# Kernel tuning notes

Measured on AMD Instinct MI355X. Metric: run time of the kernel, lower is better.

The kernel has to match this reference:

```python
import jax, jax.numpy as jnp
import numpy as np

B, C, H, W = 4, 256, 48, 48
HEADS, DH = 8, 32
INNER = HEADS * DH
HID = 128  # max(16, INNER//2)
SCALE = DH ** -0.5
EPS = 1e-6


def setup_inputs() -> dict:
    key = jax.random.key(0)
    ks = jax.random.split(key, 32)
    s = 0.02
    inp = {
        'x': jax.random.normal(ks[0], (B, C, H, W), jnp.float32),
        'rgb_input': jax.random.uniform(ks[1], (B, 3, H, W), jnp.float32),
        'wq': jax.random.normal(ks[2], (INNER, C), jnp.float32) * s,
        'bq': jnp.zeros((INNER,), jnp.float32),
        'wk': jax.random.normal(ks[3], (INNER, C), jnp.float32) * s,
        'bk': jnp.zeros((INNER,), jnp.float32),
        'wv': jax.random.normal(ks[4], (INNER, C), jnp.float32) * s,
        'bv': jnp.zeros((INNER,), jnp.float32),
        'wproj': jax.random.normal(ks[5], (C, INNER), jnp.float32) * s,
        'bproj': jnp.zeros((C,), jnp.float32),
        'c1_w': jax.random.normal(ks[6], (HID, 1, 3, 3), jnp.float32) * s,
        'c1_b': jnp.zeros((HID,), jnp.float32),
        'c2_w': jax.random.normal(ks[7], (HID, HID, 3, 3), jnp.float32) * s,
        'c2_b': jnp.zeros((HID,), jnp.float32),
        'gq_w': jax.random.normal(ks[8], (INNER, HID), jnp.float32) * s,
        'gq_b': jnp.ones((INNER,), jnp.float32),
        'bqf_w': jax.random.normal(ks[9], (INNER, HID), jnp.float32) * s,
        'bqf_b': jnp.zeros((INNER,), jnp.float32),
        'gk_w': jax.random.normal(ks[10], (INNER, HID), jnp.float32) * s,
        'gk_b': jnp.ones((INNER,), jnp.float32),
        'bkf_w': jax.random.normal(ks[11], (INNER, HID), jnp.float32) * s,
        'bkf_b': jnp.zeros((INNER,), jnp.float32),
        'gv_w': jax.random.normal(ks[12], (INNER, HID), jnp.float32) * s,
        'gv_b': jnp.ones((INNER,), jnp.float32),
        'bvf_w': jax.random.normal(ks[13], (INNER, HID), jnp.float32) * s,
        'bvf_b': jnp.zeros((INNER,), jnp.float32),
        'alpha': jnp.float32(0.1),
    }
    return inp


def _conv3(x, w, b):
    y = jax.lax.conv_general_dilated(x, w, (1, 1), 'SAME',
                                     dimension_numbers=('NCHW', 'OIHW', 'NCHW'))
    return y + b[None, :, None, None]


def _rgb_to_luma(rgb):
    y = 0.299 * rgb[:, 0:1] + 0.587 * rgb[:, 1:2] + 0.114 * rgb[:, 2:3]
    y_min = jnp.min(y, axis=(2, 3), keepdims=True)
    y_max = jnp.max(y, axis=(2, 3), keepdims=True)
    return (y - y_min) / (y_max - y_min + EPS)


def reference(x, rgb_input, wq, bq, wk, bk, wv, bv, wproj, bproj,
              c1_w, c1_b, c2_w, c2_b,
              gq_w, gq_b, bqf_w, bqf_b, gk_w, gk_b, bkf_w, bkf_b,
              gv_w, gv_b, bvf_w, bvf_b, alpha):
    Bx, Cx, Hx, Wx = x.shape
    N = Hx * Wx
    luma = _rgb_to_luma(rgb_input)  # [B,1,H,W]

    # LumaCond trunk + FiLM params (1x1 convs then global spatial mean)
    h = jax.nn.relu(_conv3(luma, c1_w, c1_b))
    h = jax.nn.relu(_conv3(h, c2_w, c2_b))
    hm = h.mean(axis=(2, 3))  # [B,HID] (mean commutes with 1x1 conv)

    def film_params(gw, gb, bw, bb):
        g = hm @ gw.T + gb  # [B, INNER]
        bta = hm @ bw.T + bb
        return (g.reshape(Bx, HEADS, DH, 1), bta.reshape(Bx, HEADS, DH, 1))

    gq, fbq = film_params(gq_w, gq_b, bqf_w, bqf_b)
    gk, fbk = film_params(gk_w, gk_b, bkf_w, bkf_b)
    gv, fbv = film_params(gv_w, gv_b, bvf_w, bvf_b)

    def proj_film(w, b, g, bta):
        t = jnp.einsum('bchw,oc->bohw', x, w) + b[None, :, None, None]
        t = t.reshape(Bx, HEADS, DH, N)
        return g * t + bta  # [B,heads,dh,N]

    q = proj_film(wq, bq, gq, fbq)
    k = proj_film(wk, bk, gk, fbk)
    v = proj_film(wv, bv, gv, fbv)

    logits = jnp.einsum('bhdn,bhdm->bhnm', q, k) * SCALE  # [B,heads,N,N]

    # luma bias: avg-pooled inverse luma, mean-centered per image
    invL = 1.0 - luma
    invL = jax.lax.reduce_window(invL, 0.0, jax.lax.add,
                                 (1, 1, 3, 3), (1, 1, 1, 1), 'SAME') / 9.0
    invL = invL.reshape(Bx, N)
    invL = invL - invL.mean(axis=-1, keepdims=True)
    logits = logits + alpha * invL[:, None, None, :]

    attn = jax.nn.softmax(logits, axis=-1)
    out = jnp.einsum('bhnm,bhdm->bhdn', attn, v)  # [B,heads,dh,N]
    out = out.reshape(Bx, INNER, Hx, Wx)
    return jnp.einsum('bchw,oc->bohw', out, wproj) + bproj[None, :, None, None]
```

## Files before the change

### kernel.cpp

```cpp
#include <hip/hip_runtime.h>


#define NSP 2304
#define WID 48

typedef __attribute__((ext_vector_type(4))) float  fvec4;
typedef __attribute__((ext_vector_type(2))) unsigned int uvec2;
typedef __attribute__((ext_vector_type(4))) unsigned int uvec4;
typedef __attribute__((ext_vector_type(8))) short  short8;
typedef __attribute__((ext_vector_type(4))) float  f32x4;

__device__ inline unsigned short f2bf(float f){
  unsigned int u = __builtin_bit_cast(unsigned int, f);
  u += 0x7fffu + ((u >> 16) & 1u);
  return (unsigned short)(u >> 16);
}
__device__ inline unsigned pack2bf(float a, float b){
#if __has_builtin(__builtin_amdgcn_cvt_pk_bf16_f32)
  typedef __attribute__((ext_vector_type(2))) __bf16 bf16x2;
  bf16x2 r = __builtin_amdgcn_cvt_pk_bf16_f32(a, b);
  return __builtin_bit_cast(unsigned, r);
#else
  return (unsigned)f2bf(a) | ((unsigned)f2bf(b) << 16);
#endif
}

__global__ void k0b_wcast(const float* __restrict__ c2w, const float* __restrict__ wq,
                          const float* __restrict__ wk, const float* __restrict__ wv_,
                          const float* __restrict__ wproj,
                          unsigned short* __restrict__ wtb,
                          unsigned short* __restrict__ wqkvb,
                          unsigned short* __restrict__ wprojb){
  int idx = blockIdx.x*256 + threadIdx.x;
  if (idx < 147456){
    int ic = idx & 127, rem = idx >> 7;
    int oc = rem & 127, tap = rem >> 7;
    wtb[idx] = f2bf(c2w[(oc*128 + ic)*9 + tap]);
  } else if (idx < 344064){
    int j = idx - 147456;
    int mat = j >> 16, oc_ = j & 65535;
    const float* src = (mat == 0) ? wq : (mat == 1) ? wk : wv_;
    wqkvb[j] = f2bf(src[oc_]);
  } else {
    int j = idx - 344064;
    wprojb[j] = f2bf(wproj[j]);
  }
}

__global__ __launch_bounds__(256) void k0xt(const float* __restrict__ x,
                                            unsigned short* __restrict__ xt){
  int nt = blockIdx.x, cc = blockIdx.y, b = blockIdx.z, t = threadIdx.x;
  __shared__ unsigned short tb[64*72];
  int cl0 = t >> 4;
  int nl0 = (t & 15) * 4;
  #pragma unroll
  for (int ps = 0; ps < 4; ++ps){
    int cl = cl0 + ps*16;
    fvec4 v = *(const fvec4*)(x + ((size_t)(b*256 + cc*64 + cl))*NSP + nt*64 + nl0);
    #pragma unroll
    for (int i = 0; i < 4; ++i) tb[(nl0+i)*72 + cl] = f2bf(v[i]);
  }
  __syncthreads();
  int nl = t >> 2, cg = (t & 3) * 16;
  uvec4 u0 = *(const uvec4*)&tb[nl*72 + cg];
  uvec4 u1 = *(const uvec4*)&tb[nl*72 + cg + 8];
  unsigned short* dst = xt + ((size_t)(b*NSP + nt*64 + nl))*256 + cc*64 + cg;
  *(uvec4*)dst = u0;
  *(uvec4*)(dst + 8) = u1;
}

__global__ __launch_bounds__(1024) void k1_luma(const float* __restrict__ rgb,
                        const float* __restrict__ alphaP,
                        float* __restrict__ luma_n, float* __restrict__ bias_a,
                        float* __restrict__ hm_sum, unsigned short* __restrict__ h1p){
  int b = blockIdx.x, t = threadIdx.x;
  __shared__ float ly[NSP];
  __shared__ float ll[NSP];
  __shared__ float red[1024];
  __shared__ float red2[1024];
  {
    const uvec4 z = {0u,0u,0u,0u};
    for (int j = t; j < 196*16; j += 1024){
      int cell = j >> 4, q = j & 15;
      int r, c;
      if (cell < 50)      { r = 0;           c = cell; }
      else if (cell < 100){ r = 49;          c = cell - 50; }
      else if (cell < 148){ r = cell - 99;   c = 0; }
      else                { r = cell - 147;  c = 49; }
      *(uvec4*)(h1p + ((size_t)(b*2500 + r*50 + c))*128 + q*8) = z;
    }
  }
  const float* rp = rgb + b*3*NSP;
  float lmin = 1e30f, lmax = -1e30f;
  for (int i = t; i < NSP; i += 1024){
    float y = 0.299f*rp[i] + 0.587f*rp[NSP+i] + 0.114f*rp[2*NSP+i];
    ly[i] = y; lmin = fminf(lmin, y); lmax = fmaxf(lmax, y);
  }
  red[t] = lmin; red2[t] = lmax;
  __syncthreads();
  for (int s = 512; s > 0; s >>= 1){
    if (t < s){ red[t] = fminf(red[t], red[t+s]); red2[t] = fmaxf(red2[t], red2[t+s]); }
    __syncthreads();
  }
  float mn = red[0], mx = red2[0];
  float inv = 1.0f / (mx - mn + 1e-6f);
  for (int i = t; i < NSP; i += 1024){
    float v = (ly[i] - mn) * inv;
    ll[i] = v;
    luma_n[b*NSP + i] = v;
  }
  if (t < 128) hm_sum[b*128 + t] = 0.f;
  __syncthreads();
  float pr[3]; float psum = 0.f;
  #pragma unroll
  for (int ii = 0; ii < 3; ++ii){
    int n = t + 1024*ii;
    pr[ii] = 0.f;
    if (n < NSP){
      int row = n / WID, col = n - row*WID;
      float s = 0.f;
      #pragma unroll
      for (int dy = -1; dy <= 1; ++dy)
        #pragma unroll
        for (int dx = -1; dx <= 1; ++dx){
          int r2 = row+dy, c2 = col+dx;
          if (r2 >= 0 && r2 < WID && c2 >= 0 && c2 < WID) s += 1.0f - ll[r2*WID + c2];
        }
      pr[ii] = s * (1.f/9.f);
      psum += pr[ii];
    }
  }
  __syncthreads();
  red[t] = psum;
  __syncthreads();
  for (int s = 512; s > 0; s >>= 1){
    if (t < s) red[t] += red[t+s];
    __syncthreads();
  }
  float mean = red[0] * (1.f/(float)NSP);
  float alpha = alphaP[0] * 1.4426950408889634f;
  #pragma unroll
  for (int ii = 0; ii < 3; ++ii){
    int n = t + 1024*ii;
    if (n < NSP) bias_a[b*NSP + n] = alpha * (pr[ii] - mean);
  }
}

__global__ void k2_conv1(const float* __restrict__ luma_n, const float* __restrict__ c1w,
                         const float* __restrict__ c1b, unsigned short* __restrict__ h1p){
  int nt = blockIdx.x, ocg = blockIdx.y, b = blockIdx.z, t = threadIdx.x;
  __shared__ float wsm[32*9];
  __shared__ float bsm[32];
  for (int i = t; i < 288; i += 256) wsm[i] = c1w[ocg*288 + i];
  if (t < 32) bsm[t] = c1b[ocg*32 + t];
  __syncthreads();
  int n = nt*256 + t;
  int row = n / WID, col = n - row*WID;
  const float* lp = luma_n + b*NSP;
  float lv[9];
  int k = 0;
  #pragma unroll
  for (int dy = -1; dy <= 1; ++dy)
    #pragma unroll
    for (int dx = -1; dx <= 1; ++dx, ++k){
      int r2 = row+dy, c2 = col+dx;
      lv[k] = (r2 >= 0 && r2 < WID && c2 >= 0 && c2 < WID) ? lp[r2*WID + c2] : 0.f;
    }
  unsigned int packed[16];
  #pragma unroll
  for (int oc2 = 0; oc2 < 16; ++oc2){
    float a0 = bsm[oc2*2], a1 = bsm[oc2*2+1];
    #pragma unroll
    for (int q = 0; q < 9; ++q){
      a0 += wsm[(oc2*2)*9 + q] * lv[q];
      a1 += wsm[(oc2*2+1)*9 + q] * lv[q];
    }
    packed[oc2] = pack2bf(fmaxf(a0, 0.f), fmaxf(a1, 0.f));
  }
  unsigned short* dst = h1p + ((size_t)(b*2500 + (row+1)*50 + (col+1)))*128 + ocg*32;
  #pragma unroll
  for (int q4 = 0; q4 < 4; ++q4)
    *(uvec4*)(dst + q4*8) = *(uvec4*)&packed[q4*4];
}

__global__ __launch_bounds__(256) void k3_conv2(const unsigned short* __restrict__ h1p,
    const unsigned short* __restrict__ wtb, const float* __restrict__ c2b,
    float* __restrict__ hm_sum){
  int row = blockIdx.x, mh = blockIdx.y, b = blockIdx.z;
  int t = threadIdx.x, wv = t >> 6, lane = t & 63;
  int lq = lane >> 4, lc = lane & 15;
  int ocb = mh*64 + wv*16;
  const f32x4 z4 = {0.f, 0.f, 0.f, 0.f};
  f32x4 C[3] = {z4, z4, z4};
  const unsigned short* hbase = h1p + (size_t)b*2500*128;
  #pragma unroll
  for (int tap = 0; tap < 9; ++tap){
    int dy = tap/3 - 1, dx = tap%3 - 1;
    const unsigned short* wrow = wtb + (tap*128 + ocb + lc)*128 + lq*8;
    const unsigned short* hrow = hbase + ((row+dy+1)*50 + (dx+1) + lc)*128 + lq*8;
    #pragma unroll
    for (int kc = 0; kc < 4; ++kc){
      short8 aW = *(const short8*)(wrow + kc*32);
      #pragma unroll
      for (int ntp = 0; ntp < 3; ++ntp){
        short8 bH = *(const short8*)(hrow + ntp*16*128 + kc*32);
        C[ntp] = __builtin_amdgcn_mfma_f32_16x16x32_bf16(aW, bH, C[ntp], 0, 0, 0);
      }
    }
  }
  float s[4];
  #pragma unroll
  for (int r = 0; r < 4; ++r){
    float bias = c2b[ocb + lq*4 + r];
    float v = 0.f;
    #pragma unroll
    for (int ntp = 0; ntp < 3; ++ntp) v += fmaxf(C[ntp][r] + bias, 0.f);
    v += __shfl_xor(v, 1, 64);
    v += __shfl_xor(v, 2, 64);
    v += __shfl_xor(v, 4, 64);
    v += __shfl_xor(v, 8, 64);
    s[r] = v;
  }
  if (lc == 0){
    #pragma unroll
    for (int r = 0; r < 4; ++r)
      atomicAdd(&hm_sum[b*128 + ocb + lq*4 + r], s[r]);
  }
}

__global__ void k4_film(const float* __restrict__ hm_sum,
  const float* w0, const float* b0, const float* w1, const float* b1,
  const float* w2, const float* b2, const float* w3, const float* b3,
  const float* w4, const float* b4, const float* w5, const float* b5,
  float* __restrict__ film){
  __shared__ float hs[128];
  int bb = blockIdx.x & 3, m6 = blockIdx.x >> 2, t = threadIdx.x;
  if (t < 128) hs[t] = hm_sum[bb*128 + t] * (1.f/(float)NSP);
  __syncthreads();
  const float* wm[6] = {w0,w1,w2,w3,w4,w5};
  const float* bm[6] = {b0,b1,b2,b3,b4,b5};
  const float* w = wm[m6];
  int o = t;
  float a = bm[m6][o];
  for (int h2 = 0; h2 < 128; ++h2) a += hs[h2] * w[o*128 + h2];
  film[blockIdx.x*256 + t] = a;
}

__global__ __launch_bounds__(256) void k5_qkv(const unsigned short* __restrict__ xt,
    const unsigned short* __restrict__ wqkvb,
    const float* __restrict__ bq, const float* __restrict__ bk, const float* __restrict__ bv,
    const float* __restrict__ film,
    unsigned short* __restrict__ q_t, unsigned short* __restrict__ k_t,
    unsigned short* __restrict__ v_b){
  int nt = blockIdx.x, ot = blockIdx.y, b = blockIdx.z;
  int t = threadIdx.x, wv = t >> 6, lane = t & 63;
  int lq = lane >> 4, lc = lane & 15;
  int p = ot >> 1;
  int omb = (ot & 1)*128 + wv*32;
  const f32x4 z4 = {0.f, 0.f, 0.f, 0.f};
  f32x4 acc[2][4];
  #pragma unroll
  for (int oh = 0; oh < 2; ++oh)
    #pragma unroll
    for (int nq = 0; nq < 4; ++nq) acc[oh][nq] = z4;

  const unsigned short* wbp = wqkvb + p*65536 + (omb + lc)*256 + lq*8;
  const unsigned short* xbp = xt + ((size_t)(b*NSP + nt*64 + lc))*256 + lq*8;

  short8 aW0[2], aW1[2], bX0[4], bX1[4];
  auto loadW = [&](short8 (&W)[2], int kc){
    #pragma unroll
    for (int oh = 0; oh < 2; ++oh) W[oh] = *(const short8*)(wbp + oh*16*256 + kc*32);
  };
  auto loadX = [&](short8 (&X)[4], int kc){
    #pragma unroll
    for (int nq = 0; nq < 4; ++nq) X[nq] = *(const short8*)(xbp + (size_t)nq*16*256 + kc*32);
  };
  auto mm = [&](short8 (&W)[2], short8 (&X)[4]){
    #pragma unroll
    for (int oh = 0; oh < 2; ++oh)
      #pragma unroll
      for (int nq = 0; nq < 4; ++nq)
        acc[oh][nq] = __builtin_amdgcn_mfma_f32_16x16x32_bf16(W[oh], X[nq], acc[oh][nq], 0, 0, 0);
  };
  loadW(aW0, 0); loadX(bX0, 0);
  for (int kc2 = 0; kc2 < 4; ++kc2){
    loadW(aW1, kc2*2+1); loadX(bX1, kc2*2+1);
    mm(aW0, bX0);
    int kn = (kc2*2+2) & 7;
    loadW(aW0, kn); loadX(bX0, kn);
    mm(aW1, bX1);
  }

  const float* bvec = (p == 0) ? bq : (p == 1) ? bk : bv;
  int hq = omb >> 5;
  unsigned short* qk = (p == 0) ? q_t : k_t;
  #pragma unroll
  for (int oh = 0; oh < 2; ++oh){
    fvec4 g4 = *(const fvec4*)(film + (2*p*4 + b)*256 + omb + oh*16 + lq*4);
    fvec4 t4 = *(const fvec4*)(film + ((2*p+1)*4 + b)*256 + omb + oh*16 + lq*4);
    fvec4 z4b = *(const fvec4*)(bvec + omb + oh*16 + lq*4);
    #pragma unroll
    for (int nq = 0; nq < 4; ++nq){
      int n = nt*64 + nq*16 + lc;
      float v0 = g4[0]*(acc[oh][nq][0] + z4b[0]) + t4[0];
      float v1 = g4[1]*(acc[oh][nq][1] + z4b[1]) + t4[1];
      float v2 = g4[2]*(acc[oh][nq][2] + z4b[2]) + t4[2];
      float v3 = g4[3]*(acc[oh][nq][3] + z4b[3]) + t4[3];
      if (p == 0){
        const float sc = 0.17677669529663687f * 1.4426950408889634f;
        v0 *= sc; v1 *= sc; v2 *= sc; v3 *= sc;
      }
      if (p < 2){
        uvec2 u;
        u.x = pack2bf(v0, v1);
        u.y = pack2bf(v2, v3);
        *(uvec2*)(qk + ((size_t)((b*8 + hq)*NSP + n))*32 + oh*16 + lq*4) = u;
      } else {
        int om = omb + oh*16 + lq*4;
        v_b[((size_t)(b*256 + om + 0))*NSP + n] = f2bf(v0);
        v_b[((size_t)(b*256 + om + 1))*NSP + n] = f2bf(v1);
        v_b[((size_t)(b*256 + om + 2))*NSP + n] = f2bf(v2);
        v_b[((size_t)(b*256 + om + 3))*NSP + n] = f2bf(v3);
      }
    }
  }
}

__global__ __launch_bounds__(256, 4) void k6_attn(const unsigned short* __restrict__ q_t,
    const unsigned short* __restrict__ k_t, const unsigned short* __restrict__ v_b,
    const float* __restrict__ bias_a,
    unsigned short* __restrict__ o0, unsigned short* __restrict__ o1,
    float* __restrict__ l0, float* __restrict__ l1){
  int bx = blockIdx.x, h = blockIdx.y, b = blockIdx.z;
  int qblk = bx >> 1, s = bx & 1;
  unsigned short* op = s ? o1 : o0;
  float* lp = s ? l1 : l0;
  int t = threadIdx.x, wv = t >> 6, lane = t & 63;
  int lq = lane >> 4, lc = lane & 15;
  int bh = b*8 + h;
  int nb0 = qblk*128 + wv*32;
  const f32x4 z4 = {0.f, 0.f, 0.f, 0.f};
  int ms = s*1152;

  __shared__ unsigned short Kb[2][64*32];
  __shared__ unsigned short Vb[2][32*64];
  __shared__ float ps[4][1024];
  float* myps = ps[wv];
  int sxm = ((lc&7)<<2) | (((lc>>3)&1)<<1);
  int wbase = lc*32;

  const unsigned short* kg = k_t + ((size_t)(bh*NSP + ms + (t>>2)))*32 + (t&3)*8;
  const unsigned short* vg = v_b + ((size_t)(b*256 + h*32 + (t>>3)))*NSP + ms + (t&7)*8;
  int krow = t >> 2;
  unsigned short* kw = &Kb[0][krow*32 + (((t&3) ^ ((krow>>1)&3))*8)];
  int vrow = t >> 3;
  unsigned short* vw = &Vb[0][vrow*64 + (((t&7) ^ (vrow&7))*8)];

  int kcol = (lq ^ ((lc>>1)&3))*8;

  const float* brow = bias_a + b*NSP + ms;

  short8 aQ[2];
  #pragma unroll
  for (int qf = 0; qf < 2; ++qf)
    aQ[qf] = *(const short8*)(q_t + ((size_t)(bh*NSP + nb0 + qf*16 + lc))*32 + lq*8);

  fvec4 c0r[4];
  #pragma unroll
  for (int g = 0; g < 4; ++g) c0r[g] = *(const fvec4*)(brow + g*16 + lq*4);

  const uvec4 onesu = {0x3F803F80u, 0x3F803F80u, 0x3F803F80u, 0x3F803F80u};
  const short8 aOnes = __builtin_bit_cast(short8, onesu);

  f32x4 O[2][2]; f32x4 Ol[2];
  #pragma unroll
  for (int qf = 0; qf < 2; ++qf){
    Ol[qf] = z4; O[qf][0] = z4; O[qf][1] = z4;
  }

  short8 aK[4], aV[2][2], bP[2][2];

  auto readP = [&](){
    #pragma unroll
    for (int qf = 0; qf < 2; ++qf)
      #pragma unroll
      for (int mh = 0; mh < 2; ++mh){
        int d0 = (mh*16 + lq*4) ^ sxm;
        uvec2 lo = *(const uvec2*)&myps[qf*512 + wbase + d0];
        uvec2 hi = *(const uvec2*)&myps[qf*512 + wbase + (d0 ^ 2)];
        uvec4 up; up.x = lo.x; up.y = lo.y; up.z = hi.x; up.w = hi.y;
        bP[qf][mh] = __builtin_bit_cast(short8, up);
      }
  };
  auto sphase = [&](){
    #pragma unroll
    for (int qf = 0; qf < 2; ++qf){
      #pragma unroll
      for (int g = 0; g < 4; ++g){
        f32x4 S = __builtin_amdgcn_mfma_f32_16x16x32_bf16(aK[g], aQ[qf], c0r[g], 0, 0, 0);
        uvec2 w2;
        w2.x = pack2bf(__builtin_amdgcn_exp2f(S[0]), __builtin_amdgcn_exp2f(S[1]));
        w2.y = pack2bf(__builtin_amdgcn_exp2f(S[2]), __builtin_amdgcn_exp2f(S[3]));
        *(uvec2*)&myps[qf*512 + wbase + ((g*8 + lq*2) ^ sxm)] = w2;
      }
    }
  };
  auto pv = [&](){
    __builtin_amdgcn_s_setprio(1);
    #pragma unroll
    for (int qf = 0; qf < 2; ++qf){
      #pragma unroll
      for (int mh = 0; mh < 2; ++mh){
        Ol[qf] = __builtin_amdgcn_mfma_f32_16x16x32_bf16(aOnes, bP[qf][mh], Ol[qf], 0, 0, 0);
        #pragma unroll
        for (int dhg = 0; dhg < 2; ++dhg)
          O[qf][dhg] = __builtin_amdgcn_mfma_f32_16x16x32_bf16(aV[dhg][mh], bP[qf][mh], O[qf][dhg], 0, 0, 0);
      }
    }
    __builtin_amdgcn_s_setprio(0);
  };

  uvec4 gKr = *(const uvec4*)kg;
  uvec4 gVr = *(const uvec4*)vg;

  for (int it = 0; it < 18; ++it){
    int buf = it & 1;
    *(uvec4*)(kw + buf*2048) = gKr;
    *(uvec4*)(vw + buf*2048) = gVr;
    __syncthreads();
    if (it < 17){
      gKr = *(const uvec4*)(kg + (size_t)(it+1)*2048);
      gVr = *(const uvec4*)(vg + (it+1)*64);
    }
    const unsigned short* kb = Kb[buf];
    #pragma unroll
    for (int g = 0; g < 4; ++g)
      aK[g] = *(const short8*)(kb + (g*16 + lc)*32 + kcol);
    if (it > 0) readP();
    sphase();
    if (it < 17){
      #pragma unroll
      for (int g = 0; g < 4; ++g)
        c0r[g] = *(const fvec4*)(brow + (it+1)*64 + g*16 + lq*4);
    }
    if (it > 0) pv();
    const unsigned short* vb = Vb[buf];
    #pragma unroll
    for (int dhg = 0; dhg < 2; ++dhg)
      #pragma unroll
      for (int mh = 0; mh < 2; ++mh)
        aV[dhg][mh] = *(const short8*)(vb + (dhg*16 + lc)*64 + (((mh*4 + lq) ^ (lc&7))*8));
  }
  readP();
  pv();

  #pragma unroll
  for (int qf = 0; qf < 2; ++qf){
    int nidx = nb0 + qf*16 + lc;
    if (lq == 0) lp[b*NSP + nidx] = Ol[qf][0];
    #pragma unroll
    for (int dh = 0; dh < 2; ++dh){
      uvec2 u;
      u.x = pack2bf(O[qf][dh][0], O[qf][dh][1]);
      u.y = pack2bf(O[qf][dh][2], O[qf][dh][3]);
      *(uvec2*)(op + ((size_t)(b*NSP + nidx))*256 + h*32 + dh*16 + lq*4) = u;
    }
  }
}

__global__ __launch_bounds__(256) void k7_proj(const unsigned short* __restrict__ a0,
    const unsigned short* __restrict__ a1, const float* __restrict__ l0p,
    const float* __restrict__ l1p, const unsigned short* __restrict__ wprojb,
    const float* __restrict__ bproj, float* __restrict__ out){
  int nt = blockIdx.x, ct = blockIdx.y, b = blockIdx.z;
  int t = threadIdx.x, wv = t >> 6, lane = t & 63;
  int lq = lane >> 4, lc = lane & 15;
  __shared__ float rls[32];
  if (t < 32) rls[t] = 1.0f / (l0p[b*NSP + nt*32 + t] + l1p[b*NSP + nt*32 + t]);
  __syncthreads();
  int cb = ct*128 + wv*32;
  const f32x4 z4 = {0.f, 0.f, 0.f, 0.f};
  f32x4 acc[2][2];
  #pragma unroll
  for (int ch = 0; ch < 2; ++ch)
    #pragma unroll
    for (int nq = 0; nq < 2; ++nq) acc[ch][nq] = z4;

  const unsigned short* wpp = wprojb + (cb + lc)*256 + lq*8;
  const unsigned short* a0p = a0 + ((size_t)(b*NSP + nt*32 + lc))*256 + lq*8;
  const unsigned short* a1p = a1 + ((size_t)(b*NSP + nt*32 + lc))*256 + lq*8;

  short8 W0[2], W1[2], p00[2], p01[2], p10[2], p11[2];
  auto loadS = [&](short8 (&W)[2], short8 (&B0)[2], short8 (&B1)[2], int kc){
    #pragma unroll
    for (int ch = 0; ch < 2; ++ch) W[ch] = *(const short8*)(wpp + ch*16*256 + kc*32);
    #pragma unroll
    for (int nq = 0; nq < 2; ++nq){
      B0[nq] = *(const short8*)(a0p + (size_t)nq*16*256 + kc*32);
      B1[nq] = *(const short8*)(a1p + (size_t)nq*16*256 + kc*32);
    }
  };
  auto mmS = [&](short8 (&W)[2], short8 (&B0)[2], short8 (&B1)[2]){
    #pragma unroll
    for (int ch = 0; ch < 2; ++ch)
      #pragma unroll
      for (int nq = 0; nq < 2; ++nq){
        acc[ch][nq] = __builtin_amdgcn_mfma_f32_16x16x32_bf16(W[ch], B0[nq], acc[ch][nq], 0, 0, 0);
        acc[ch][nq] = __builtin_amdgcn_mfma_f32_16x16x32_bf16(W[ch], B1[nq], acc[ch][nq], 0, 0, 0);
      }
  };
  loadS(W0, p00, p10, 0);
  for (int kc2 = 0; kc2 < 4; ++kc2){
    loadS(W1, p01, p11, kc2*2+1);
    mmS(W0, p00, p10);
    int kn = (kc2*2+2) & 7;
    loadS(W0, p00, p10, kn);
    mmS(W1, p01, p11);
  }

  #pragma unroll
  for (int ch = 0; ch < 2; ++ch){
    #pragma unroll
    for (int nq = 0; nq < 2; ++nq){
      int n = nt*32 + nq*16 + lc;
      float rl = rls[nq*16 + lc];
      #pragma unroll
      for (int r = 0; r < 4; ++r){
        int c = cb + ch*16 + lq*4 + r;
        out[((size_t)(b*256 + c))*NSP + n] = acc[ch][nq][r]*rl + bproj[c];
      }
    }
  }
}

extern "C" void kernel_launch(void* const* d_in, const int* in_sizes, int n_in,
                              void* d_out, int out_size, void* d_ws, size_t ws_size,
                              hipStream_t stream) {
  const float* x     = (const float*)d_in[0];
  const float* rgb   = (const float*)d_in[1];
  const float* wq    = (const float*)d_in[2];
  const float* bq    = (const float*)d_in[3];
  const float* wk    = (const float*)d_in[4];
  const float* bk    = (const float*)d_in[5];
  const float* wv    = (const float*)d_in[6];
  const float* bv    = (const float*)d_in[7];
  const float* wproj = (const float*)d_in[8];
  const float* bproj = (const float*)d_in[9];
  const float* c1w   = (const float*)d_in[10];
  const float* c1b   = (const float*)d_in[11];
  const float* c2w   = (const float*)d_in[12];
  const float* c2b   = (const float*)d_in[13];
  const float* gq_w  = (const float*)d_in[14];
  const float* gq_b  = (const float*)d_in[15];
  const float* bqf_w = (const float*)d_in[16];
  const float* bqf_b = (const float*)d_in[17];
  const float* gk_w  = (const float*)d_in[18];
  const float* gk_b  = (const float*)d_in[19];
  const float* bkf_w = (const float*)d_in[20];
  const float* bkf_b = (const float*)d_in[21];
  const float* gv_w  = (const float*)d_in[22];
  const float* gv_b  = (const float*)d_in[23];
  const float* bvf_w = (const float*)d_in[24];
  const float* bvf_b = (const float*)d_in[25];
  const float* alphaP= (const float*)d_in[26];

  char* w = (char*)d_ws;
  float* luma_n = (float*)w;            w += 4*NSP*4;
  float* bias_a = (float*)w;            w += 4*NSP*4;
  float* hm_sum = (float*)w;            w += 512*4;
  float* film   = (float*)w;            w += 6*4*256*4;
  unsigned short* h1p = (unsigned short*)w; w += 4*2500*128*2;
  unsigned short* wtb = (unsigned short*)w; w += 9*128*128*2;
  unsigned short* wqkvb = (unsigned short*)w; w += 3*256*256*2;
  unsigned short* wprojb = (unsigned short*)w; w += 256*256*2;
  unsigned short* xt  = (unsigned short*)w; w += (size_t)4*NSP*256*2;
  unsigned short* q_t = (unsigned short*)w; w += (size_t)4*8*NSP*32*2;
  unsigned short* k_t = (unsigned short*)w; w += (size_t)4*8*NSP*32*2;
  unsigned short* v_b = (unsigned short*)w; w += (size_t)4*256*NSP*2;
  unsigned short* o_part0 = (unsigned short*)w; w += (size_t)4*NSP*256*2;
  unsigned short* o_part1 = (unsigned short*)w; w += (size_t)4*NSP*256*2;
  float* l_part0 = (float*)w;           w += 4*NSP*4;
  float* l_part1 = (float*)w;           w += 4*NSP*4;

  k0b_wcast<<<1600, 256, 0, stream>>>(c2w, wq, wk, wv, wproj, wtb, wqkvb, wprojb);
  k0xt    <<<dim3(36,4,4), 256, 0, stream>>>(x, xt);
  k1_luma <<<4, 1024, 0, stream>>>(rgb, alphaP, luma_n, bias_a, hm_sum, h1p);
  k2_conv1<<<dim3(9,4,4), 256, 0, stream>>>(luma_n, c1w, c1b, h1p);
  k3_conv2<<<dim3(48,2,4), 256, 0, stream>>>(h1p, wtb, c2b, hm_sum);
  k4_film <<<24, 256, 0, stream>>>(hm_sum, gq_w, gq_b, bqf_w, bqf_b,
                                   gk_w, gk_b, bkf_w, bkf_b,
                                   gv_w, gv_b, bvf_w, bvf_b, film);
  k5_qkv  <<<dim3(36,6,4), 256, 0, stream>>>(xt, wqkvb, bq, bk, bv, film,
                                             q_t, k_t, v_b);
  k6_attn <<<dim3(36,8,4), 256, 0, stream>>>(q_t, k_t, v_b, bias_a,
                                             o_part0, o_part1, l_part0, l_part1);
  k7_proj <<<dim3(72,2,4), 256, 0, stream>>>(o_part0, o_part1, l_part0, l_part1,
                                             wprojb, bproj, (float*)d_out);
}
```

Baseline: 278.0 us.

## Merge three prep kernels into one launch and de-pipeline attention PV loop

Combines the weight cast, x transpose and luma/bias kernels into a single block-indexed prep kernel, with luma now handled by 256-thread blocks, to save two launches and let the pieces run concurrently. The attention loop is also restructured: the software-pipelined P readback and PV MFMA (which consumed the previous iteration's P) are replaced by doing score, P write, P read and PV in the same iteration. This removes the cross-iteration overlap and lowers register pressure. The luma blocks now run with fewer threads, so that part may take longer, and the attention loop loses its latency hiding.

```diff
diff --git a/kernel.cpp b/kernel.cpp
--- a/kernel.cpp
+++ b/kernel.cpp
@@ -25,124 +25,120 @@
 #endif
 }
 
-__global__ void k0b_wcast(const float* __restrict__ c2w, const float* __restrict__ wq,
-                          const float* __restrict__ wk, const float* __restrict__ wv_,
-                          const float* __restrict__ wproj,
-                          unsigned short* __restrict__ wtb,
-                          unsigned short* __restrict__ wqkvb,
-                          unsigned short* __restrict__ wprojb){
-  int idx = blockIdx.x*256 + threadIdx.x;
-  if (idx < 147456){
-    int ic = idx & 127, rem = idx >> 7;
-    int oc = rem & 127, tap = rem >> 7;
-    wtb[idx] = f2bf(c2w[(oc*128 + ic)*9 + tap]);
-  } else if (idx < 344064){
-    int j = idx - 147456;
-    int mat = j >> 16, oc_ = j & 65535;
-    const float* src = (mat == 0) ? wq : (mat == 1) ? wk : wv_;
-    wqkvb[j] = f2bf(src[oc_]);
-  } else {
-    int j = idx - 344064;
-    wprojb[j] = f2bf(wproj[j]);
-  }
-}
-
-__global__ __launch_bounds__(256) void k0xt(const float* __restrict__ x,
-                                            unsigned short* __restrict__ xt){
-  int nt = blockIdx.x, cc = blockIdx.y, b = blockIdx.z, t = threadIdx.x;
-  __shared__ unsigned short tb[64*72];
-  int cl0 = t >> 4;
-  int nl0 = (t & 15) * 4;
-  #pragma unroll
-  for (int ps = 0; ps < 4; ++ps){
-    int cl = cl0 + ps*16;
-    fvec4 v = *(const fvec4*)(x + ((size_t)(b*256 + cc*64 + cl))*NSP + nt*64 + nl0);
-    #pragma unroll
-    for (int i = 0; i < 4; ++i) tb[(nl0+i)*72 + cl] = f2bf(v[i]);
-  }
-  __syncthreads();
-  int nl = t >> 2, cg = (t & 3) * 16;
-  uvec4 u0 = *(const uvec4*)&tb[nl*72 + cg];
-  uvec4 u1 = *(const uvec4*)&tb[nl*72 + cg + 8];
-  unsigned short* dst = xt + ((size_t)(b*NSP + nt*64 + nl))*256 + cc*64 + cg;
-  *(uvec4*)dst = u0;
-  *(uvec4*)(dst + 8) = u1;
-}
-
-__global__ __launch_bounds__(1024) void k1_luma(const float* __restrict__ rgb,
-                        const float* __restrict__ alphaP,
-                        float* __restrict__ luma_n, float* __restrict__ bias_a,
-                        float* __restrict__ hm_sum, unsigned short* __restrict__ h1p){
-  int b = blockIdx.x, t = threadIdx.x;
-  __shared__ float ly[NSP];
-  __shared__ float ll[NSP];
-  __shared__ float red[1024];
-  __shared__ float red2[1024];
-  {
-    const uvec4 z = {0u,0u,0u,0u};
-    for (int j = t; j < 196*16; j += 1024){
-      int cell = j >> 4, q = j & 15;
-      int r, c;
-      if (cell < 50)      { r = 0;           c = cell; }
-      else if (cell < 100){ r = 49;          c = cell - 50; }
-      else if (cell < 148){ r = cell - 99;   c = 0; }
-      else                { r = cell - 147;  c = 49; }
-      *(uvec4*)(h1p + ((size_t)(b*2500 + r*50 + c))*128 + q*8) = z;
-    }
-  }
-  const float* rp = rgb + b*3*NSP;
-  float lmin = 1e30f, lmax = -1e30f;
-  for (int i = t; i < NSP; i += 1024){
-    float y = 0.299f*rp[i] + 0.587f*rp[NSP+i] + 0.114f*rp[2*NSP+i];
-    ly[i] = y; lmin = fminf(lmin, y); lmax = fmaxf(lmax, y);
-  }
-  red[t] = lmin; red2[t] = lmax;
-  __syncthreads();
-  for (int s = 512; s > 0; s >>= 1){
-    if (t < s){ red[t] = fminf(red[t], red[t+s]); red2[t] = fmaxf(red2[t], red2[t+s]); }
+__global__ __launch_bounds__(256) void k_prep(const float* __restrict__ c2w,
+    const float* __restrict__ wq, const float* __restrict__ wk, const float* __restrict__ wv_,
+    const float* __restrict__ wproj, const float* __restrict__ x,
+    const float* __restrict__ rgb, const float* __restrict__ alphaP,
+    unsigned short* __restrict__ wtb, unsigned short* __restrict__ wqkvb,
+    unsigned short* __restrict__ wprojb, unsigned short* __restrict__ xt,
+    float* __restrict__ luma_n, float* __restrict__ bias_a,
+    float* __restrict__ hm_sum, unsigned short* __restrict__ h1p){
+  __shared__ __align__(16) float sm[5120];
+  int bx = blockIdx.x, t = threadIdx.x;
+  if (bx < 4){
+    int b = bx;
+    float* ly  = sm;
+    float* ll  = sm + NSP;
+    float* red = sm + 2*NSP;
+    float* red2= sm + 2*NSP + 256;
+    {
+      const uvec4 z = {0u,0u,0u,0u};
+      for (int j = t; j < 196*16; j += 256){
+        int cell = j >> 4, q = j & 15;
+        int r, c;
+        if (cell < 50)      { r = 0;           c = cell; }
+        else if (cell < 100){ r = 49;          c = cell - 50; }
+        else if (cell < 148){ r = cell - 99;   c = 0; }
+        else                { r = cell - 147;  c = 49; }
+        *(uvec4*)(h1p + ((size_t)(b*2500 + r*50 + c))*128 + q*8) = z;
+      }
+    }
+    const float* rp = rgb + b*3*NSP;
+    float lmin = 1e30f, lmax = -1e30f;
+    for (int i = t; i < NSP; i += 256){
+      float y = 0.299f*rp[i] + 0.587f*rp[NSP+i] + 0.114f*rp[2*NSP+i];
+      ly[i] = y; lmin = fminf(lmin, y); lmax = fmaxf(lmax, y);
+    }
+    red[t] = lmin; red2[t] = lmax;
     __syncthreads();
-  }
-  float mn = red[0], mx = red2[0];
-  float inv = 1.0f / (mx - mn + 1e-6f);
-  for (int i = t; i < NSP; i += 1024){
-    float v = (ly[i] - mn) * inv;
-    ll[i] = v;
-    luma_n[b*NSP + i] = v;
-  }
-  if (t < 128) hm_sum[b*128 + t] = 0.f;
-  __syncthreads();
-  float pr[3]; float psum = 0.f;
-  #pragma unroll
-  for (int ii = 0; ii < 3; ++ii){
-    int n = t + 1024*ii;
-    pr[ii] = 0.f;
-    if (n < NSP){
+    for (int s = 128; s > 0; s >>= 1){
+      if (t < s){ red[t] = fminf(red[t], red[t+s]); red2[t] = fmaxf(red2[t], red2[t+s]); }
+      __syncthreads();
+    }
+    float mn = red[0], mx = red2[0];
+    float inv = 1.0f / (mx - mn + 1e-6f);
+    for (int i = t; i < NSP; i += 256){
+      float v = (ly[i] - mn) * inv;
+      ll[i] = v;
+      luma_n[b*NSP + i] = v;
+    }
+    if (t < 128) hm_sum[b*128 + t] = 0.f;
+    __syncthreads();
+    float pr[9]; float psum = 0.f;
+    #pragma unroll
+    for (int ii = 0; ii < 9; ++ii){
+      int n = t + 256*ii;
       int row = n / WID, col = n - row*WID;
-      float s = 0.f;
+      float s2 = 0.f;
       #pragma unroll
       for (int dy = -1; dy <= 1; ++dy)
         #pragma unroll
         for (int dx = -1; dx <= 1; ++dx){
           int r2 = row+dy, c2 = col+dx;
-          if (r2 >= 0 && r2 < WID && c2 >= 0 && c2 < WID) s += 1.0f - ll[r2*WID + c2];
+          if (r2 >= 0 && r2 < WID && c2 >= 0 && c2 < WID) s2 += 1.0f - ll[r2*WID + c2];
         }
-      pr[ii] = s * (1.f/9.f);
+      pr[ii] = s2 * (1.f/9.f);
       psum += pr[ii];
     }
-  }
-  __syncthreads();
-  red[t] = psum;
-  __syncthreads();
-  for (int s = 512; s > 0; s >>= 1){
-    if (t < s) red[t] += red[t+s];
     __syncthreads();
-  }
-  float mean = red[0] * (1.f/(float)NSP);
-  float alpha = alphaP[0] * 1.4426950408889634f;
-  #pragma unroll
-  for (int ii = 0; ii < 3; ++ii){
-    int n = t + 1024*ii;
-    if (n < NSP) bias_a[b*NSP + n] = alpha * (pr[ii] - mean);
+    red[t] = psum;
+    __syncthreads();
+    for (int s = 128; s > 0; s >>= 1){
+      if (t < s) red[t] += red[t+s];
+      __syncthreads();
+    }
+    float mean = red[0] * (1.f/(float)NSP);
+    float alpha = alphaP[0] * 1.4426950408889634f;
+    #pragma unroll
+    for (int ii = 0; ii < 9; ++ii){
+      int n = t + 256*ii;
+      bias_a[b*NSP + n] = alpha * (pr[ii] - mean);
+    }
+  } else if (bx < 1604){
+    int idx = (bx - 4)*256 + t;
+    if (idx < 147456){
+      int ic = idx & 127, rem = idx >> 7;
+      int oc = rem & 127, tap = rem >> 7;
+      wtb[idx] = f2bf(c2w[(oc*128 + ic)*9 + tap]);
+    } else if (idx < 344064){
+      int j = idx - 147456;
+      int mat = j >> 16, oc_ = j & 65535;
+      const float* src = (mat == 0) ? wq : (mat == 1) ? wk : wv_;
+      wqkvb[j] = f2bf(src[oc_]);
+    } else {
+      int j = idx - 344064;
+      wprojb[j] = f2bf(wproj[j]);
+    }
+  } else {
+    int j = bx - 1604;
+    int nt = j % 36, cc = (j / 36) & 3, b = j / 144;
+    unsigned short* tb = (unsigned short*)sm;
+    int cl0 = t >> 4;
+    int nl0 = (t & 15) * 4;
+    #pragma unroll
+    for (int ps_ = 0; ps_ < 4; ++ps_){
+      int cl = cl0 + ps_*16;
+      fvec4 v = *(const fvec4*)(x + ((size_t)(b*256 + cc*64 + cl))*NSP + nt*64 + nl0);
+      #pragma unroll
+      for (int i = 0; i < 4; ++i) tb[(nl0+i)*72 + cl] = f2bf(v[i]);
+    }
+    __syncthreads();
+    int nl = t >> 2, cg = (t & 3) * 16;
+    uvec4 u0 = *(const uvec4*)&tb[nl*72 + cg];
+    uvec4 u1 = *(const uvec4*)&tb[nl*72 + cg + 8];
+    unsigned short* dst = xt + ((size_t)(b*NSP + nt*64 + nl))*256 + cc*64 + cg;
+    *(uvec4*)dst = u0;
+    *(uvec4*)(dst + 8) = u1;
   }
 }
 
@@ -346,11 +342,8 @@
   __shared__ unsigned short Kb[2][64*32];
   __shared__ unsigned short Vb[2][32*64];
   __shared__ float ps[4][1024];
-  float* myps = ps[wv];
-  int sxm = ((lc&7)<<2) | (((lc>>3)&1)<<1);
-  int wbase = lc*32;
-
-  const unsigned short* kg = k_t + ((size_t)(bh*NSP + ms + (t>>2)))*32 + (t&3)*8;
+
+  const unsigned short* kg = k_t + ((size_t)bh*NSP + ms + (t>>2))*32 + (t&3)*8;
   const unsigned short* vg = v_b + ((size_t)(b*256 + h*32 + (t>>3)))*NSP + ms + (t&7)*8;
   int krow = t >> 2;
   unsigned short* kw = &Kb[0][krow*32 + (((t&3) ^ ((krow>>1)&3))*8)];
@@ -358,17 +351,21 @@
   unsigned short* vw = &Vb[0][vrow*64 + (((t&7) ^ (vrow&7))*8)];
 
   int kcol = (lq ^ ((lc>>1)&3))*8;
+  int sxm = ((lc&7)<<2) | (((lc>>3)&1)<<1);
+  int wbase = lc*32;
 
   const float* brow = bias_a + b*NSP + ms;
+  fvec4 c0r[4];
+  #pragma unroll
+  for (int g = 0; g < 4; ++g) c0r[g] = *(const fvec4*)(brow + g*16 + lq*4);
 
   short8 aQ[2];
   #pragma unroll
   for (int qf = 0; qf < 2; ++qf)
     aQ[qf] = *(const short8*)(q_t + ((size_t)(bh*NSP + nb0 + qf*16 + lc))*32 + lq*8);
 
-  fvec4 c0r[4];
-  #pragma unroll
-  for (int g = 0; g < 4; ++g) c0r[g] = *(const fvec4*)(brow + g*16 + lq*4);
+  uvec4 gKr = *(const uvec4*)kg;
+  uvec4 gVr = *(const uvec4*)vg;
 
   const uvec4 onesu = {0x3F803F80u, 0x3F803F80u, 0x3F803F80u, 0x3F803F80u};
   const short8 aOnes = __builtin_bit_cast(short8, onesu);
@@ -378,22 +375,28 @@
   for (int qf = 0; qf < 2; ++qf){
     Ol[qf] = z4; O[qf][0] = z4; O[qf][1] = z4;
   }
-
-  short8 aK[4], aV[2][2], bP[2][2];
-
-  auto readP = [&](){
-    #pragma unroll
-    for (int qf = 0; qf < 2; ++qf)
-      #pragma unroll
-      for (int mh = 0; mh < 2; ++mh){
-        int d0 = (mh*16 + lq*4) ^ sxm;
-        uvec2 lo = *(const uvec2*)&myps[qf*512 + wbase + d0];
-        uvec2 hi = *(const uvec2*)&myps[qf*512 + wbase + (d0 ^ 2)];
-        uvec4 up; up.x = lo.x; up.y = lo.y; up.z = hi.x; up.w = hi.y;
-        bP[qf][mh] = __builtin_bit_cast(short8, up);
-      }
-  };
-  auto sphase = [&](){
+  float* myps = ps[wv];
+
+  for (int it = 0; it < 18; ++it){
+    int buf = it & 1;
+    *(uvec4*)(kw + buf*2048) = gKr;
+    *(uvec4*)(vw + buf*2048) = gVr;
+    __syncthreads();
+    if (it < 17){
+      gKr = *(const uvec4*)(kg + (it+1)*2048);
+      gVr = *(const uvec4*)(vg + (it+1)*64);
+    }
+    const unsigned short* kb = Kb[buf];
+    const unsigned short* vb = Vb[buf];
+    short8 aK[4], aV[2][2];
+    #pragma unroll
+    for (int g = 0; g < 4; ++g)
+      aK[g] = *(const short8*)(kb + (g*16 + lc)*32 + kcol);
+    #pragma unroll
+    for (int dhg = 0; dhg < 2; ++dhg)
+      #pragma unroll
+      for (int mh = 0; mh < 2; ++mh)
+        aV[dhg][mh] = *(const short8*)(vb + (dhg*16 + lc)*64 + (((mh*4 + lq) ^ (lc&7))*8));
     #pragma unroll
     for (int qf = 0; qf < 2; ++qf){
       #pragma unroll
@@ -405,56 +408,29 @@
         *(uvec2*)&myps[qf*512 + wbase + ((g*8 + lq*2) ^ sxm)] = w2;
       }
     }
-  };
-  auto pv = [&](){
+    if (it < 17){
+      #pragma unroll
+      for (int g = 0; g < 4; ++g)
+        c0r[g] = *(const fvec4*)(brow + (it+1)*64 + g*16 + lq*4);
+    }
     __builtin_amdgcn_s_setprio(1);
     #pragma unroll
     for (int qf = 0; qf < 2; ++qf){
       #pragma unroll
       for (int mh = 0; mh < 2; ++mh){
-        Ol[qf] = __builtin_amdgcn_mfma_f32_16x16x32_bf16(aOnes, bP[qf][mh], Ol[qf], 0, 0, 0);
+        int d0 = (mh*16 + lq*4) ^ sxm;
+        uvec2 lo = *(const uvec2*)&myps[qf*512 + wbase + d0];
+        uvec2 hi = *(const uvec2*)&myps[qf*512 + wbase + (d0 ^ 2)];
+        uvec4 up; up.x = lo.x; up.y = lo.y; up.z = hi.x; up.w = hi.y;
+        short8 bP = __builtin_bit_cast(short8, up);
+        Ol[qf] = __builtin_amdgcn_mfma_f32_16x16x32_bf16(aOnes, bP, Ol[qf], 0, 0, 0);
         #pragma unroll
         for (int dhg = 0; dhg < 2; ++dhg)
-          O[qf][dhg] = __builtin_amdgcn_mfma_f32_16x16x32_bf16(aV[dhg][mh], bP[qf][mh], O[qf][dhg], 0, 0, 0);
+          O[qf][dhg] = __builtin_amdgcn_mfma_f32_16x16x32_bf16(aV[dhg][mh], bP, O[qf][dhg], 0, 0, 0);
       }
     }
     __builtin_amdgcn_s_setprio(0);
-  };
-
-  uvec4 gKr = *(const uvec4*)kg;
-  uvec4 gVr = *(const uvec4*)vg;
-
-  for (int it = 0; it < 18; ++it){
-    int buf = it & 1;
-    *(uvec4*)(kw + buf*2048) = gKr;
-    *(uvec4*)(vw + buf*2048) = gVr;
-    __syncthreads();
-    if (it < 17){
-      gKr = *(const uvec4*)(kg + (size_t)(it+1)*2048);
-      gVr = *(const uvec4*)(vg + (it+1)*64);
-    }
-    const unsigned short* kb = Kb[buf];
-    #pragma unroll
-    for (int g = 0; g < 4; ++g)
-      aK[g] = *(const short8*)(kb + (g*16 + lc)*32 + kcol);
-    if (it > 0) readP();
-    sphase();
-    if (it < 17){
-      #pragma unroll
-      for (int g = 0; g < 4; ++g)
-        c0r[g] = *(const fvec4*)(brow + (it+1)*64 + g*16 + lq*4);
-    }
-    if (it > 0) pv();
-    const unsigned short* vb = Vb[buf];
-    #pragma unroll
-    for (int dhg = 0; dhg < 2; ++dhg)
-      #pragma unroll
-      for (int mh = 0; mh < 2; ++mh)
-        aV[dhg][mh] = *(const short8*)(vb + (dhg*16 + lc)*64 + (((mh*4 + lq) ^ (lc&7))*8));
-  }
-  readP();
-  pv();
-
+  }
   #pragma unroll
   for (int qf = 0; qf < 2; ++qf){
     int nidx = nb0 + qf*16 + lc;
@@ -583,9 +559,9 @@
   float* l_part0 = (float*)w;           w += 4*NSP*4;
   float* l_part1 = (float*)w;           w += 4*NSP*4;
 
-  k0b_wcast<<<1600, 256, 0, stream>>>(c2w, wq, wk, wv, wproj, wtb, wqkvb, wprojb);
-  k0xt    <<<dim3(36,4,4), 256, 0, stream>>>(x, xt);
-  k1_luma <<<4, 1024, 0, stream>>>(rgb, alphaP, luma_n, bias_a, hm_sum, h1p);
+  k_prep  <<<2180, 256, 0, stream>>>(c2w, wq, wk, wv, wproj, x, rgb, alphaP,
+                                     wtb, wqkvb, wprojb, xt,
+                                     luma_n, bias_a, hm_sum, h1p);
   k2_conv1<<<dim3(9,4,4), 256, 0, stream>>>(luma_n, c1w, c1b, h1p);
   k3_conv2<<<dim3(48,2,4), 256, 0, stream>>>(h1p, wtb, c2b, hm_sum);
   k4_film <<<24, 256, 0, stream>>>(hm_sum, gq_w, gq_b, bqf_w, bqf_b,
```

After: 261.0 us (median of 2 runs). -6.1%, faster.
